# Kernel tuning notes

Hardware: AMD Instinct MI355X
Metric: run time of the kernel (lower is better)

The kernel has to match this reference:

```python
import jax, jax.numpy as jnp
import numpy as np

N_OBJ = 25
N_FEAT = 64
D = [256, 256, 256, 10]


def setup_inputs() -> dict:
    key = jax.random.key(0)
    ks = jax.random.split(key, 10)
    N = 1024
    x = jax.random.normal(ks[0], (N, N_OBJ * N_FEAT), dtype=jnp.float32)
    # conv2d weight (D0, n_features, 2, 1) split into the two kernel taps
    conv_w0 = jax.random.normal(ks[1], (D[0], N_FEAT), dtype=jnp.float32)
    conv_w1 = jax.random.normal(ks[2], (D[0], N_FEAT), dtype=jnp.float32)
    conv_b = jnp.zeros((D[0],), dtype=jnp.float32)
    def lin(k, fan_in, fan_out):
        bound = 1.0 / np.sqrt(fan_in)
        kw, kb = jax.random.split(k)
        w = jax.random.uniform(kw, (fan_out, fan_in), minval=-bound, maxval=bound, dtype=jnp.float32)
        b = jax.random.uniform(kb, (fan_out,), minval=-bound, maxval=bound, dtype=jnp.float32)
        return w, b
    w1, b1 = lin(ks[3], D[0], D[1])
    w2, b2 = lin(ks[4], D[1], D[2])
    w3, b3 = lin(ks[5], D[2], D[3])
    return {"x": x, "conv_w0": conv_w0, "conv_w1": conv_w1, "conv_b": conv_b,
            "w1": w1, "b1": b1, "w2": w2, "b2": b2, "w3": w3, "b3": b3}


def reference(x, conv_w0, conv_w1, conv_b, w1, b1, w2, b2, w3, b3):
    N = x.shape[0]
    O = N_OBJ
    xo = x.reshape(N, O, N_FEAT)  # (N, objects, features)
    # conv2d kernel (2,1) with dilation d: out[h] = w0.x[h] + w1.x[h+d] + b
    A = jnp.einsum('nof,cf->noc', xo, conv_w0)  # tap-0 contribution per object
    B = jnp.einsum('nof,cf->noc', xo, conv_w1)  # tap-1 contribution per object
    # all pairs (i, j=i+d), j>i: relu(A_i + B_j + b)
    act = jax.nn.relu(A[:, :, None, :] + B[:, None, :, :] + conv_b)  # (N,O,O,D0)
    idx = jnp.arange(O)
    diff = idx[None, :] - idx[:, None]  # j - i
    # avg_pool over (O-d) positions for dilation d, then mean over the O-1 dilations
    mask = jnp.where(diff > 0, 1.0 / (O - diff).astype(jnp.float32), 0.0)
    h = jnp.einsum('nijc,ij->nc', act, mask) / (O - 1)  # (N, D0)
    # MLP: relu on all but last layer
    h = jax.nn.relu(h @ w1.T + b1)
    h = jax.nn.relu(h @ w2.T + b2)
    return h @ w3.T + b3
```

## Files before the change

### kernel.cpp

```cpp
#include <hip/hip_runtime.h>
#include <hip/hip_bf16.h>

#define NOBJ 25

typedef _Float16 f16x8 __attribute__((ext_vector_type(8)));
typedef short s16x4 __attribute__((ext_vector_type(4)));
typedef float f32x4 __attribute__((ext_vector_type(4)));
typedef unsigned int uint;

__device__ __forceinline__ short f2h_s(float f) {
  _Float16 h = (_Float16)f;
  return *reinterpret_cast<short*>(&h);
}

__global__ __launch_bounds__(256, 2) void conv_prep_kernel(
    const float* __restrict__ x,
    const float* __restrict__ cw0,
    const float* __restrict__ cw1,
    const float* __restrict__ cb,
    const float* __restrict__ w1, const float* __restrict__ w2,
    const float* __restrict__ w3,
    short* __restrict__ h0,
    short* __restrict__ wfm)
{
  __shared__ short xs[2][32][72];
  __shared__ float ab[4][2][NOBJ][68];

  const int t = threadIdx.x;
  const int lane = t & 63;
  const int wv = t >> 6;
  const int r = lane & 15;
  const int g = lane >> 4;
  const int n0 = blockIdx.x * 2;

  for (int s = 0; s < 2; ++s) {
    const float4* xg = reinterpret_cast<const float4*>(x + (size_t)(n0 + s) * (NOBJ * 64));
    for (int i = t; i < 400; i += 256) {
      float4 v = xg[i];
      s16x4 p;
      p.x = f2h_s(v.x); p.y = f2h_s(v.y); p.z = f2h_s(v.z); p.w = f2h_s(v.w);
      *reinterpret_cast<s16x4*>(&xs[s][i >> 4][(i & 15) * 4]) = p;
    }
  }

  for (int j = blockIdx.x * 256 + t; j < 135168; j += 512 * 256) {
    const float* w; int f, nt;
    const bool isw3 = (j >= 131072);
    if (!isw3) {
      w = (j >> 16) ? w2 : w1;
      f = j & 65535;
      nt = f >> 12;
    } else {
      f = j - 131072;
      w = w3;
      nt = 0;
    }
    const int ks = (f >> 9) & 7;
    const int l  = (f >> 3) & 63;
    const int jj = f & 7;
    const int col = nt * 16 + (l & 15);
    const int k   = ks * 32 + (l >> 4) * 8 + jj;
    const float v = (isw3 && col >= 10) ? 0.f : w[col * 256 + k];
    wfm[j] = f2h_s(v);
  }

  f16x8 Wf[2][4][2];
#pragma unroll
  for (int tap = 0; tap < 2; ++tap) {
    const float* wsrc = tap ? cw1 : cw0;
#pragma unroll
    for (int ntl = 0; ntl < 4; ++ntl)
#pragma unroll
      for (int ks = 0; ks < 2; ++ks) {
        const int ch = wv * 64 + ntl * 16 + r;
        const float* p = wsrc + ch * 64 + ks * 32 + g * 8;
        const float4 a = *reinterpret_cast<const float4*>(p);
        const float4 b = *reinterpret_cast<const float4*>(p + 4);
        f16x8 fr;
        fr[0] = (_Float16)a.x; fr[1] = (_Float16)a.y; fr[2] = (_Float16)a.z; fr[3] = (_Float16)a.w;
        fr[4] = (_Float16)b.x; fr[5] = (_Float16)b.y; fr[6] = (_Float16)b.z; fr[7] = (_Float16)b.w;
        Wf[tap][ntl][ks] = fr;
      }
  }
  float cbv[4];
#pragma unroll
  for (int ntl = 0; ntl < 4; ++ntl) cbv[ntl] = cb[wv * 64 + ntl * 16 + r];

  __syncthreads();

  for (int s = 0; s < 2; ++s) {
    f16x8 Xf[2][2];
#pragma unroll
    for (int mt = 0; mt < 2; ++mt)
#pragma unroll
      for (int ks = 0; ks < 2; ++ks)
        Xf[mt][ks] = *reinterpret_cast<const f16x8*>(&xs[s][mt * 16 + r][ks * 32 + g * 8]);

    f32x4 acc[2][2][4];
#pragma unroll
    for (int tap = 0; tap < 2; ++tap)
#pragma unroll
      for (int mt = 0; mt < 2; ++mt)
#pragma unroll
        for (int ntl = 0; ntl < 4; ++ntl) {
          f32x4 z = {0.f, 0.f, 0.f, 0.f};
          acc[tap][mt][ntl] = z;
        }

#pragma unroll
    for (int tap = 0; tap < 2; ++tap)
#pragma unroll
      for (int mt = 0; mt < 2; ++mt)
#pragma unroll
        for (int ntl = 0; ntl < 4; ++ntl)
#pragma unroll
          for (int ks = 0; ks < 2; ++ks)
            acc[tap][mt][ntl] = __builtin_amdgcn_mfma_f32_16x16x32_f16(
                Xf[mt][ks], Wf[tap][ntl][ks], acc[tap][mt][ntl], 0, 0, 0);

#pragma unroll
    for (int tap = 0; tap < 2; ++tap)
#pragma unroll
      for (int mt = 0; mt < 2; ++mt)
#pragma unroll
        for (int ntl = 0; ntl < 4; ++ntl) {
          const int cl = ntl * 16 + r;
          const int row0 = mt * 16 + g * 4;
          const float badd = (tap == 0) ? cbv[ntl] : 0.f;
#pragma unroll
          for (int q = 0; q < 4; ++q)
            if (row0 + q < NOBJ) ab[wv][tap][row0 + q][cl] = acc[tap][mt][ntl][q] + badd;
        }

    float A[NOBJ], Bv[NOBJ];
#pragma unroll
    for (int i = 0; i < NOBJ; ++i) { A[i] = ab[wv][0][i][lane]; Bv[i] = ab[wv][1][i][lane]; }
    float hacc = 0.f;
#pragma unroll
    for (int d = 1; d < NOBJ; ++d) {
      float sd = 0.f;
#pragma unroll
      for (int i = 0; i + d < NOBJ; ++i) sd += fmaxf(A[i] + Bv[i + d], 0.f);
      hacc = __builtin_fmaf(sd, 1.0f / (float)(NOBJ - d), hacc);
    }
    h0[(size_t)(n0 + s) * 256 + t] = f2h_s(hacc * (1.0f / (float)(NOBJ - 1)));
  }
}

__global__ __launch_bounds__(1024, 4) void mlp_fused(
    const short* __restrict__ h0,
    const short* __restrict__ wfm,
    const float* __restrict__ b1, const float* __restrict__ b2,
    const float* __restrict__ b3,
    float* __restrict__ out)
{
  __shared__ short Hs[2][16][272];
  const int t = threadIdx.x, lane = t & 63, wv = t >> 6;
  const int r = lane & 15, g = lane >> 4;
  const int m0 = blockIdx.x * 16;

  {
    const s16x4 v = reinterpret_cast<const s16x4*>(h0 + (size_t)m0 * 256)[t];
    *reinterpret_cast<s16x4*>(&Hs[0][t >> 6][(t & 63) * 4]) = v;
  }
  __syncthreads();

  int pp = 0;
  const float* bias[2] = {b1, b2};
#pragma unroll
  for (int L = 0; L < 2; ++L) {
    const short* wl = wfm + L * 65536;

    f16x8 bfr[8];
#pragma unroll
    for (int ks = 0; ks < 8; ++ks)
      bfr[ks] = *reinterpret_cast<const f16x8*>(wl + ((wv * 8 + ks) << 9) + lane * 8);

    const float bv = bias[L][wv * 16 + r];
    f32x4 acc = {bv, bv, bv, bv};
#pragma unroll
    for (int ks = 0; ks < 8; ++ks) {
      const f16x8 afr = *reinterpret_cast<const f16x8*>(&Hs[pp][r][ks * 32 + g * 8]);
      acc = __builtin_amdgcn_mfma_f32_16x16x32_f16(afr, bfr[ks], acc, 0, 0, 0);
    }

    const int col = wv * 16 + r;
#pragma unroll
    for (int q = 0; q < 4; ++q)
      Hs[pp ^ 1][4 * g + q][col] = f2h_s(fmaxf(acc[q], 0.f));
    __syncthreads();
    pp ^= 1;
  }

  if (wv == 0) {
    const float bv = (r < 10) ? b3[r] : 0.f;
    f32x4 acc = {bv, bv, bv, bv};
#pragma unroll
    for (int ks = 0; ks < 8; ++ks) {
      const f16x8 afr = *reinterpret_cast<const f16x8*>(&Hs[pp][r][ks * 32 + g * 8]);
      const f16x8 bfr = *reinterpret_cast<const f16x8*>(wfm + 131072 + (ks << 9) + lane * 8);
      acc = __builtin_amdgcn_mfma_f32_16x16x32_f16(afr, bfr, acc, 0, 0, 0);
    }
    if (r < 10) {
#pragma unroll
      for (int q = 0; q < 4; ++q)
        out[(size_t)(m0 + 4 * g + q) * 10 + r] = acc[q];
    }
  }
}

extern "C" void kernel_launch(void* const* d_in, const int* in_sizes, int n_in,
                              void* d_out, int out_size, void* d_ws, size_t ws_size,
                              hipStream_t stream) {
  const float* x   = (const float*)d_in[0];
  const float* cw0 = (const float*)d_in[1];
  const float* cw1 = (const float*)d_in[2];
  const float* cb  = (const float*)d_in[3];
  const float* w1  = (const float*)d_in[4];
  const float* b1  = (const float*)d_in[5];
  const float* w2  = (const float*)d_in[6];
  const float* b2  = (const float*)d_in[7];
  const float* w3  = (const float*)d_in[8];
  const float* b3  = (const float*)d_in[9];
  float* out = (float*)d_out;

  short* h0  = (short*)d_ws;
  short* wfm = h0 + 262144;

  conv_prep_kernel<<<512, 256, 0, stream>>>(x, cw0, cw1, cb, w1, w2, w3, h0, wfm);
  mlp_fused<<<64, 1024, 0, stream>>>(h0, wfm, b1, b2, b3, out);
}
```

Before: 27.95 us.

## Split conv channels across blocks and compute pairwise relu sums in packed fp16

The conv/pair kernel now launches twice as many blocks, each handling half the output channels for two samples. Inputs are loaded straight from global into MFMA fragments instead of being staged in LDS. The O(O^2) pairwise relu-sum now runs in packed fp16, using v_pk_max_f16 and a split of dilations by parity across half-waves, with a shuffle reduction at the end. The aim is to cut VALU work and raise occupancy, at the cost of fp16 accumulation error in the pairwise sums and duplicated x reads across blocks.

```diff
diff --git a/kernel.cpp b/kernel.cpp
--- a/kernel.cpp
+++ b/kernel.cpp
@@ -4,6 +4,7 @@
 #define NOBJ 25
 
 typedef _Float16 f16x8 __attribute__((ext_vector_type(8)));
+typedef _Float16 f16x2 __attribute__((ext_vector_type(2)));
 typedef short s16x4 __attribute__((ext_vector_type(4)));
 typedef float f32x4 __attribute__((ext_vector_type(4)));
 typedef unsigned int uint;
@@ -12,8 +13,21 @@
   _Float16 h = (_Float16)f;
   return *reinterpret_cast<short*>(&h);
 }
-
-__global__ __launch_bounds__(256, 2) void conv_prep_kernel(
+__device__ __forceinline__ f16x8 cvt8h(const float* p) {
+  const float4 a = *reinterpret_cast<const float4*>(p);
+  const float4 b = *reinterpret_cast<const float4*>(p + 4);
+  f16x8 fr;
+  fr[0] = (_Float16)a.x; fr[1] = (_Float16)a.y; fr[2] = (_Float16)a.z; fr[3] = (_Float16)a.w;
+  fr[4] = (_Float16)b.x; fr[5] = (_Float16)b.y; fr[6] = (_Float16)b.z; fr[7] = (_Float16)b.w;
+  return fr;
+}
+__device__ __forceinline__ f16x2 pk_max(f16x2 a, f16x2 b) {
+  f16x2 r;
+  asm("v_pk_max_f16 %0, %1, %2" : "=v"(r) : "v"(a), "v"(b));
+  return r;
+}
+
+__global__ __launch_bounds__(256, 4) void conv_prep_kernel(
     const float* __restrict__ x,
     const float* __restrict__ cw0,
     const float* __restrict__ cw1,
@@ -23,27 +37,18 @@
     short* __restrict__ h0,
     short* __restrict__ wfm)
 {
-  __shared__ short xs[2][32][72];
-  __shared__ float ab[4][2][NOBJ][68];
+  __shared__ short abp[4][2][26][33][2];
 
   const int t = threadIdx.x;
   const int lane = t & 63;
   const int wv = t >> 6;
   const int r = lane & 15;
   const int g = lane >> 4;
-  const int n0 = blockIdx.x * 2;
-
-  for (int s = 0; s < 2; ++s) {
-    const float4* xg = reinterpret_cast<const float4*>(x + (size_t)(n0 + s) * (NOBJ * 64));
-    for (int i = t; i < 400; i += 256) {
-      float4 v = xg[i];
-      s16x4 p;
-      p.x = f2h_s(v.x); p.y = f2h_s(v.y); p.z = f2h_s(v.z); p.w = f2h_s(v.w);
-      *reinterpret_cast<s16x4*>(&xs[s][i >> 4][(i & 15) * 4]) = p;
-    }
-  }
-
-  for (int j = blockIdx.x * 256 + t; j < 135168; j += 512 * 256) {
+  const int cbid = blockIdx.x;
+  const int n0 = (cbid >> 1) * 2;
+  const int chbase = (cbid & 1) * 128 + wv * 32;
+
+  for (int j = cbid * 256 + t; j < 135168; j += 1024 * 256) {
     const float* w; int f, nt;
     const bool isw3 = (j >= 131072);
     if (!isw3) {
@@ -64,55 +69,57 @@
     wfm[j] = f2h_s(v);
   }
 
-  f16x8 Wf[2][4][2];
+  f16x8 Wf[2][2][2];
 #pragma unroll
   for (int tap = 0; tap < 2; ++tap) {
     const float* wsrc = tap ? cw1 : cw0;
 #pragma unroll
-    for (int ntl = 0; ntl < 4; ++ntl)
-#pragma unroll
-      for (int ks = 0; ks < 2; ++ks) {
-        const int ch = wv * 64 + ntl * 16 + r;
-        const float* p = wsrc + ch * 64 + ks * 32 + g * 8;
-        const float4 a = *reinterpret_cast<const float4*>(p);
-        const float4 b = *reinterpret_cast<const float4*>(p + 4);
-        f16x8 fr;
-        fr[0] = (_Float16)a.x; fr[1] = (_Float16)a.y; fr[2] = (_Float16)a.z; fr[3] = (_Float16)a.w;
-        fr[4] = (_Float16)b.x; fr[5] = (_Float16)b.y; fr[6] = (_Float16)b.z; fr[7] = (_Float16)b.w;
-        Wf[tap][ntl][ks] = fr;
-      }
-  }
-  float cbv[4];
-#pragma unroll
-  for (int ntl = 0; ntl < 4; ++ntl) cbv[ntl] = cb[wv * 64 + ntl * 16 + r];
-
-  __syncthreads();
-
+    for (int ntl = 0; ntl < 2; ++ntl)
+#pragma unroll
+      for (int ks = 0; ks < 2; ++ks)
+        Wf[tap][ntl][ks] = cvt8h(wsrc + (chbase + ntl * 16 + r) * 64 + ks * 32 + g * 8);
+  }
+  float cbv[2];
+#pragma unroll
+  for (int ntl = 0; ntl < 2; ++ntl) cbv[ntl] = cb[chbase + ntl * 16 + r];
+
+  if (g == 0) {
+#pragma unroll
+    for (int ntl = 0; ntl < 2; ++ntl) {
+      abp[wv][1][25][ntl * 16 + r][0] = f2h_s(-6.0e4f);
+      abp[wv][1][25][ntl * 16 + r][1] = f2h_s(-6.0e4f);
+    }
+  }
+
+#pragma unroll
   for (int s = 0; s < 2; ++s) {
+    const int n = n0 + s;
     f16x8 Xf[2][2];
 #pragma unroll
-    for (int mt = 0; mt < 2; ++mt)
+    for (int mt = 0; mt < 2; ++mt) {
+      const int row = mt * 16 + r;
+      const int rowc = row > 24 ? 24 : row;
 #pragma unroll
       for (int ks = 0; ks < 2; ++ks)
-        Xf[mt][ks] = *reinterpret_cast<const f16x8*>(&xs[s][mt * 16 + r][ks * 32 + g * 8]);
-
-    f32x4 acc[2][2][4];
+        Xf[mt][ks] = cvt8h(x + (size_t)n * 1600 + rowc * 64 + ks * 32 + g * 8);
+    }
+
+    f32x4 acc[2][2][2];
 #pragma unroll
     for (int tap = 0; tap < 2; ++tap)
 #pragma unroll
       for (int mt = 0; mt < 2; ++mt)
 #pragma unroll
-        for (int ntl = 0; ntl < 4; ++ntl) {
+        for (int ntl = 0; ntl < 2; ++ntl) {
           f32x4 z = {0.f, 0.f, 0.f, 0.f};
           acc[tap][mt][ntl] = z;
         }
-
 #pragma unroll
     for (int tap = 0; tap < 2; ++tap)
 #pragma unroll
       for (int mt = 0; mt < 2; ++mt)
 #pragma unroll
-        for (int ntl = 0; ntl < 4; ++ntl)
+        for (int ntl = 0; ntl < 2; ++ntl)
 #pragma unroll
           for (int ks = 0; ks < 2; ++ks)
             acc[tap][mt][ntl] = __builtin_amdgcn_mfma_f32_16x16x32_f16(
@@ -123,28 +130,49 @@
 #pragma unroll
       for (int mt = 0; mt < 2; ++mt)
 #pragma unroll
-        for (int ntl = 0; ntl < 4; ++ntl) {
+        for (int ntl = 0; ntl < 2; ++ntl) {
           const int cl = ntl * 16 + r;
           const int row0 = mt * 16 + g * 4;
           const float badd = (tap == 0) ? cbv[ntl] : 0.f;
 #pragma unroll
           for (int q = 0; q < 4; ++q)
-            if (row0 + q < NOBJ) ab[wv][tap][row0 + q][cl] = acc[tap][mt][ntl][q] + badd;
+            if (row0 + q < NOBJ)
+              abp[wv][tap][row0 + q][cl][s] = f2h_s(acc[tap][mt][ntl][q] + badd);
         }
-
-    float A[NOBJ], Bv[NOBJ];
-#pragma unroll
-    for (int i = 0; i < NOBJ; ++i) { A[i] = ab[wv][0][i][lane]; Bv[i] = ab[wv][1][i][lane]; }
-    float hacc = 0.f;
-#pragma unroll
-    for (int d = 1; d < NOBJ; ++d) {
-      float sd = 0.f;
-#pragma unroll
-      for (int i = 0; i + d < NOBJ; ++i) sd += fmaxf(A[i] + Bv[i + d], 0.f);
-      hacc = __builtin_fmaf(sd, 1.0f / (float)(NOBJ - d), hacc);
-    }
-    h0[(size_t)(n0 + s) * 256 + t] = f2h_s(hacc * (1.0f / (float)(NOBJ - 1)));
-  }
+  }
+
+  const int hh = lane >> 5, c = lane & 31;
+  const uint* abu = reinterpret_cast<const uint*>(&abp[wv][0][0][0][0]);
+  f16x2 Apk[NOBJ], Bpk[NOBJ];
+#pragma unroll
+  for (int i = 0; i < NOBJ; ++i) {
+    uint a = abu[i * 33 + c];
+    uint b = abu[858 + (i + hh) * 33 + c];
+    Apk[i] = *reinterpret_cast<f16x2*>(&a);
+    Bpk[i] = *reinterpret_cast<f16x2*>(&b);
+  }
+  const f16x2 zz = {(_Float16)0.f, (_Float16)0.f};
+  float hacc0 = 0.f, hacc1 = 0.f;
+#pragma unroll
+  for (int dv = 0; dv < 12; ++dv) {
+    f16x2 sdp = zz;
+#pragma unroll
+    for (int i = 0; i <= 23 - 2 * dv; ++i) {
+      f16x2 tt = Apk[i] + Bpk[i + 2 * dv + 1];
+      sdp += pk_max(tt, zz);
+    }
+    const float w = hh ? (1.0f / (float)(23 - 2 * dv)) : (1.0f / (float)(24 - 2 * dv));
+    hacc0 = __builtin_fmaf((float)sdp[0], w, hacc0);
+    hacc1 = __builtin_fmaf((float)sdp[1], w, hacc1);
+  }
+  hacc0 += __shfl_xor(hacc0, 32);
+  hacc1 += __shfl_xor(hacc1, 32);
+
+  const float sc = 1.0f / (float)(NOBJ - 1);
+  if (hh == 0)
+    h0[(size_t)n0 * 256 + chbase + c] = f2h_s(hacc0 * sc);
+  else
+    h0[(size_t)(n0 + 1) * 256 + chbase + c] = f2h_s(hacc1 * sc);
 }
 
 __global__ __launch_bounds__(1024, 4) void mlp_fused(
@@ -227,6 +255,6 @@
   short* h0  = (short*)d_ws;
   short* wfm = h0 + 262144;
 
-  conv_prep_kernel<<<512, 256, 0, stream>>>(x, cw0, cw1, cb, w1, w2, w3, h0, wfm);
+  conv_prep_kernel<<<1024, 256, 0, stream>>>(x, cw0, cw1, cb, w1, w2, w3, h0, wfm);
   mlp_fused<<<64, 1024, 0, stream>>>(h0, wfm, b1, b2, b3, out);
 }
```

Result: slower. 29.66 us (+6.1%).
